# Kernel tuning notes

Hardware: AMD Instinct MI355X
Metric: run time of the kernel (lower is better)

Reference implementation:

```python
import jax, jax.numpy as jnp
import numpy as np

N = 100000   # nodes per layer
E = 600000   # edges per block
FIN = 256    # raw feature dim
H = 128      # hidden_size
C = 47       # n_classes
L = 3        # num_layers = n_layers + 1
NOUT = 10000 # seed nodes
GEN_EPS = 1e-7
T = 1.0
LN_EPS = 1e-5


def setup_inputs() -> dict:
    key = jax.random.key(0)
    ks = jax.random.split(key, 10)
    return {
        "x": jax.random.normal(ks[0], (N, FIN), jnp.float32),
        "src": jax.random.randint(ks[1], (L - 1, E), 0, N),
        "dst": jax.random.randint(ks[2], (L - 1, E), 0, N),
        "node_map": jax.random.randint(ks[3], (L - 1, N), 0, N),
        "final_map": jax.random.randint(ks[4], (NOUT,), 0, N),
        "enc_w": jax.random.normal(ks[5], (FIN, H), jnp.float32) * 0.05,
        "enc_b": jnp.zeros((H,), jnp.float32),
        "gcn_w": jax.random.normal(ks[6], (L, H, H), jnp.float32) * 0.05,
        "gcn_b": jnp.zeros((L, H), jnp.float32),
        "ln_g": jnp.ones((L, H), jnp.float32),
        "ln_b": jnp.zeros((L, H), jnp.float32),
        "pred_w": jax.random.normal(ks[7], (H, C), jnp.float32) * 0.05,
        "pred_b": jnp.zeros((C,), jnp.float32),
    }


def _layer_norm(h, g, b):
    mu = jnp.mean(h, axis=-1, keepdims=True)
    var = jnp.mean(jnp.square(h - mu), axis=-1, keepdims=True)
    return (h - mu) * jax.lax.rsqrt(var + LN_EPS) * g + b


def _gen_conv(h, src, dst, w, b):
    # GENConv, aggr='softmax', mlp_layers=1, no edge_attr, no msg_norm.
    m = jax.nn.relu(h[src]) + GEN_EPS                      # [E, H] messages
    # per-destination, per-feature segment softmax with temperature T
    mx = jax.ops.segment_max(m * T, dst, num_segments=N)   # [N, H]
    e = jnp.exp(m * T - mx[dst])                           # [E, H]
    denom = jax.ops.segment_sum(e, dst, num_segments=N)    # [N, H]
    alpha = e / (denom[dst] + 1e-16)
    agg = jax.ops.segment_sum(m * alpha, dst, num_segments=N)  # [N, H]
    return (agg + h) @ w + b                               # residual + Linear (MLP)


def reference(x, src, dst, node_map, final_map, enc_w, enc_b,
              gcn_w, gcn_b, ln_g, ln_b, pred_w, pred_b):
    h = x @ enc_w + enc_b                                  # node_features_encoder
    h = _gen_conv(h, src[0], dst[0], gcn_w[0], gcn_b[0])   # gcns[0] with block-0 edges
    for layer in range(1, L):                              # res+ block
        h2 = jax.nn.relu(_layer_norm(h, ln_g[layer - 1], ln_b[layer - 1]))
        # dropout is identity in eval mode (p applied with training=False)
        # gcns[layer] uses the edge_index set BEFORE this iteration's move
        h = _gen_conv(h2, src[layer - 1], dst[layer - 1],
                      gcn_w[layer], gcn_b[layer]) + h
        h = h[node_map[layer - 1]]                         # nf_move_layer_to gather
    h = jax.nn.relu(_layer_norm(h, ln_g[L - 1], ln_b[L - 1]))
    h = h @ pred_w + pred_b                                # node_pred_linear
    h = h[final_map]                                       # seed-node extraction
    return jax.nn.log_softmax(h, axis=-1)
```

## Files before the change

kernel.cpp:

```cpp
#include <hip/hip_runtime.h>
#include <hip/hip_bf16.h>
#include <hip/hip_fp16.h>

typedef unsigned short u16;
typedef unsigned int u32;

#define N_NODES 100000
#define N_EDGES 600000
#define FIN_D   256
#define HDIM    128
#define NCLS    47
#define NOUT_D  10000
#define NCHUNK  196
#define NP2     100352
#define PCH     2048
#define PNB     ((N_EDGES + PCH - 1) / PCH)
#define EB      1024

typedef short bf16x8 __attribute__((ext_vector_type(8)));
typedef float f32x4  __attribute__((ext_vector_type(4)));

#define GPTR(p) (const __attribute__((address_space(1))) u32*)(p)
#define LPTR(p) (__attribute__((address_space(3))) u32*)(p)

__device__ __forceinline__ float bf2f(u16 u) {
    union { u32 i; float f; } v; v.i = ((u32)u) << 16; return v.f;
}
__device__ __forceinline__ u16 f2bf(float f) {
    __hip_bfloat16 h = __float2bfloat16(f);
    return *reinterpret_cast<u16*>(&h);
}
__device__ __forceinline__ float loadF(const void* p, size_t i, bool f32) {
    if (f32) return ((const float*)p)[i];
    return bf2f(((const u16*)p)[i]);
}
__device__ __forceinline__ float wave_sum(float v) {
    #pragma unroll
    for (int o = 32; o > 0; o >>= 1) v += __shfl_xor(v, o, 64);
    return v;
}
__device__ __forceinline__ float wave_max(float v) {
    #pragma unroll
    for (int o = 32; o > 0; o >>= 1) v = fmaxf(v, __shfl_xor(v, o, 64));
    return v;
}
__device__ __forceinline__ int block_excl_scan_256(int v, int* wsum) {
    int lane = threadIdx.x & 63, wv = threadIdx.x >> 6;
    int inc = v;
    #pragma unroll
    for (int off = 1; off < 64; off <<= 1) {
        int u = __shfl_up(inc, off, 64);
        if (lane >= off) inc += u;
    }
    if (lane == 63) wsum[wv] = inc;
    __syncthreads();
    if (threadIdx.x == 0) {
        int a = 0;
        #pragma unroll
        for (int w = 0; w < 4; ++w) { int t = wsum[w]; wsum[w] = a; a += t; }
    }
    __syncthreads();
    return inc - v + wsum[wv];
}

__global__ __launch_bounds__(256) void dtype_detect_kernel(
    const u16* __restrict__ x, int* __restrict__ flag)
{
    int i = blockIdx.x * 256 + threadIdx.x;
    u32 e = (x[i] >> 7) & 0xFF;
    unsigned long long b = __ballot(e >= 200);
    if ((threadIdx.x & 63) == 0) {
        int c = __popcll(b);
        if (c) atomicAdd(&flag[1], c);
    }
}

__global__ __launch_bounds__(256) void histb_kernel(
    const int* __restrict__ dst, int* __restrict__ bcnt, int ebgrid)
{
    __shared__ int h[NCHUNK];
    int half = (blockIdx.x >= ebgrid) ? 1 : 0;
    int e0 = (blockIdx.x - half * ebgrid) * EB;
    for (int i = threadIdx.x; i < NCHUNK; i += 256) h[i] = 0;
    __syncthreads();
    #pragma unroll
    for (int t = 0; t < 4; ++t) {
        int e = e0 + t * 256 + threadIdx.x;
        if (e < N_EDGES) atomicAdd(&h[dst[half * N_EDGES + e] >> 9], 1);
    }
    __syncthreads();
    for (int i = threadIdx.x; i < NCHUNK; i += 256)
        if (h[i]) atomicAdd(&bcnt[half * NCHUNK + i], h[i]);
}

__global__ __launch_bounds__(256) void coff2_kernel(
    const int* __restrict__ csum, int* __restrict__ coff,
    int* __restrict__ bcur)
{
    __shared__ int wsum[4];
    int t = threadIdx.x;
    for (int h = 0; h < 2; ++h) {
        int v = (t < NCHUNK) ? csum[h * NCHUNK + t] : 0;
        int excl = block_excl_scan_256(v, wsum);
        if (t < NCHUNK) {
            coff[h * NCHUNK + t] = excl;
            bcur[(h * NCHUNK + t) * 16] = excl;
        }
        __syncthreads();
    }
}

__global__ __launch_bounds__(256) void bucket_part_kernel(
    const int* __restrict__ src, const int* __restrict__ dst,
    const int* __restrict__ comp1,
    int* __restrict__ bcur, int2* __restrict__ tmp,
    int* __restrict__ deg2)
{
    __shared__ int hist[NCHUNK];
    __shared__ int base[NCHUNK];
    int half = (blockIdx.x >= PNB) ? 1 : 0;
    int b = blockIdx.x - half * PNB;
    int e0 = b * PCH;
    for (int i = threadIdx.x; i < NCHUNK; i += 256) hist[i] = 0;
    __syncthreads();

    int2 loc[8];
    #pragma unroll
    for (int t = 0; t < 8; ++t) {
        int e = e0 + t * 256 + threadIdx.x;
        loc[t].y = -1;
        if (e < N_EDGES) {
            int ge = half * N_EDGES + e;
            int d = dst[ge];
            int s = src[ge];
            if (half) s = comp1[s];
            loc[t] = make_int2(s, d);
            atomicAdd(&hist[d >> 9], 1);
            atomicAdd(&deg2[half * NP2 + d], 1);
        }
    }
    __syncthreads();
    for (int i = threadIdx.x; i < NCHUNK; i += 256) {
        int h = hist[i];
        base[i] = (h > 0) ? atomicAdd(&bcur[(half * NCHUNK + i) * 16], h) : 0;
        hist[i] = 0;
    }
    __syncthreads();
    #pragma unroll
    for (int t = 0; t < 8; ++t) {
        if (loc[t].y >= 0) {
            int bk = loc[t].y >> 9;
            int pos = base[bk] + atomicAdd(&hist[bk], 1);
            tmp[(size_t)half * N_EDGES + pos] = loc[t];
        }
    }
}

__global__ __launch_bounds__(256) void scan2_kernel(
    const int* __restrict__ deg2, const int* __restrict__ coff,
    int* __restrict__ rp0, int* __restrict__ rp1)
{
    __shared__ int wsum[4];
    int half = (blockIdx.x >= NCHUNK) ? 1 : 0;
    int b = blockIdx.x - half * NCHUNK;
    const int* deg = deg2 + half * NP2;
    int* rp = half ? rp1 : rp0;
    int t = threadIdx.x;
    int i0 = b * 512 + 2 * t;
    int d0 = (i0 < N_NODES) ? deg[i0] : 0;
    int d1 = (i0 + 1 < N_NODES) ? deg[i0 + 1] : 0;
    int excl = block_excl_scan_256(d0 + d1, wsum);
    int base = coff[half * NCHUNK + b] + excl;
    if (i0 < N_NODES)     rp[i0] = base;
    if (i0 + 1 < N_NODES) rp[i0 + 1] = base + d0;
    if (b == 0 && t == 0) rp[N_NODES] = N_EDGES;
}

__global__ __launch_bounds__(256) void bucket_sort_kernel(
    const int2* __restrict__ tmp,
    const int* __restrict__ rp0, const int* __restrict__ rp1,
    const int* __restrict__ coff, const int* __restrict__ csum,
    int* __restrict__ ei0, int* __restrict__ ei1)
{
    __shared__ int cur[512];
    int half = (blockIdx.x >= NCHUNK) ? 1 : 0;
    int b = blockIdx.x - half * NCHUNK;
    const int* rp = half ? rp1 : rp0;
    int* ei = half ? ei1 : ei0;
    int n0 = b * 512;
    #pragma unroll
    for (int i = threadIdx.x; i < 512; i += 256) {
        int n = n0 + i;
        cur[i] = (n < N_NODES) ? rp[n] : 0;
    }
    __syncthreads();
    int beg = coff[half * NCHUNK + b];
    int end = beg + csum[half * NCHUNK + b];
    for (int i = beg + threadIdx.x; i < end; i += 256) {
        int2 p = tmp[(size_t)half * N_EDGES + i];
        int pos = atomicAdd(&cur[p.y & 511], 1);
        ei[pos] = p.x;
    }
}

__global__ __launch_bounds__(256) void pack_b_kernel(
    const void* __restrict__ enc_w, const void* __restrict__ gcn_w,
    const int* __restrict__ dt, u16* __restrict__ Bp)
{
    const bool f32 = (dt[1] > 16);
    int o = blockIdx.x * 256 + threadIdx.x;
    if (o >= 32768 + 3 * 16384) return;
    const void* srcp; size_t soff; int m;
    if (o < 32768) { srcp = enc_w; soff = 0; m = o; }
    else {
        int l = (o - 32768) >> 14;
        srcp = gcn_w; soff = (size_t)l * 16384; m = (o - 32768) & 16383;
    }
    int j    = m & 7;
    int lane = (m >> 3) & 63;
    int ct   = (m >> 9) & 7;
    int kidx = m >> 12;
    int k = kidx * 32 + (lane >> 4) * 8 + j;
    int n = ct * 16 + (lane & 15);
    Bp[o] = f2bf(loadF(srcp, soff + (size_t)k * HDIM + n, f32));
}

__global__ __launch_bounds__(256, 2) void enc_gemm_kernel(
    const void* __restrict__ Araw, const u16* __restrict__ Bp,
    const void* __restrict__ bias, const int* __restrict__ dt,
    u16* __restrict__ OutBF)
{
    extern __shared__ char SH[];
    const bool f32 = (dt[1] > 16);
    const int tid  = threadIdx.x;
    const int w    = tid >> 6;
    const int lane = tid & 63;
    const int quad = lane >> 4;
    const int cl   = lane & 15;
    const int m0   = blockIdx.x * 16;

    #pragma unroll
    for (int i = 0; i < 16; ++i) {
        int off = (w * 16 + i) * 1024;
        __builtin_amdgcn_global_load_lds(
            GPTR((const char*)Bp + off + lane * 16),
            LPTR(SH + off), 16, 0, 0);
    }
    if (f32) {
        #pragma unroll
        for (int i = 0; i < 4; ++i) {
            int row = w * 4 + i;
            int src = (lane * 16) ^ ((row & 7) << 4);
            __builtin_amdgcn_global_load_lds(
                GPTR((const char*)Araw + (size_t)(m0 + row) * 1024 + src),
                LPTR(SH + 65536 + row * 1024), 16, 0, 0);
        }
    } else {
        #pragma unroll
        for (int i = 0; i < 2; ++i) {
            int r0 = (w * 2 + i) * 2;
            int row = r0 + (lane >> 5);
            int src = ((lane & 31) * 16) ^ ((row & 7) << 4);
            __builtin_amdgcn_global_load_lds(
                GPTR((const char*)Araw + (size_t)(m0 + row) * 512 + src),
                LPTR(SH + 65536 + r0 * 512), 16, 0, 0);
        }
    }

    f32x4 acc[2];
    acc[0] = (f32x4){0.f, 0.f, 0.f, 0.f};
    acc[1] = (f32x4){0.f, 0.f, 0.f, 0.f};
    const int ct0 = w * 2;
    const int swz = (cl & 7) << 4;

    __syncthreads();

    #pragma unroll
    for (int k = 0; k < 8; ++k) {
        bf16x8 av;
        if (f32) {
            const char* rb = SH + 65536 + cl * 1024;
            int lo = (k * 128 + quad * 32) ^ swz;
            float4 v0 = *(const float4*)(rb + lo);
            float4 v1 = *(const float4*)(rb + (lo ^ 16));
            union { u32 u[4]; bf16x8 v; } cv;
            cv.u[0] = (u32)f2bf(v0.x) | ((u32)f2bf(v0.y) << 16);
            cv.u[1] = (u32)f2bf(v0.z) | ((u32)f2bf(v0.w) << 16);
            cv.u[2] = (u32)f2bf(v1.x) | ((u32)f2bf(v1.y) << 16);
            cv.u[3] = (u32)f2bf(v1.z) | ((u32)f2bf(v1.w) << 16);
            av = cv.v;
        } else {
            const char* rb = SH + 65536 + cl * 512;
            av = *(const bf16x8*)(rb + ((k * 64 + quad * 16) ^ swz));
        }
        #pragma unroll
        for (int c = 0; c < 2; ++c) {
            bf16x8 b = *(const bf16x8*)(SH + k * 8192 + (ct0 + c) * 1024 + lane * 16);
            acc[c] = __builtin_amdgcn_mfma_f32_16x16x32_bf16(av, b, acc[c], 0, 0, 0);
        }
    }

    #pragma unroll
    for (int reg = 0; reg < 4; ++reg) {
        int grow = m0 + quad * 4 + reg;
        #pragma unroll
        for (int c = 0; c < 2; ++c) {
            int col = (ct0 + c) * 16 + cl;
            float v = acc[c][reg] + loadF(bias, col, f32);
            OutBF[(size_t)grow * HDIM + col] = f2bf(v);
        }
    }
}

template<bool OWN_MAP>
__global__ __launch_bounds__(256) void agg_msg_kernel(
    const int* __restrict__ rp, const int* __restrict__ eidx,
    const u16* __restrict__ HBin, const int* __restrict__ own_map,
    u16* __restrict__ Amsg)
{
    __shared__ u32 RS[4][16][64];
    int wave = threadIdx.x >> 6;
    int lane = threadIdx.x & 63;
    int n = blockIdx.x * 4 + wave;
    if (n >= N_NODES) return;
    const u32* HB32 = (const u32*)HBin;
    int nn = OWN_MAP ? own_map[n] : n;
    u32 own = HB32[(size_t)nn * 64 + lane];
    int beg = rp[n], end = rp[n + 1];
    float den0 = 0.f, den1 = 0.f, num0 = 0.f, num1 = 0.f;
    for (int c = beg; c < end; c += 16) {
        int cnt = end - c; if (cnt > 16) cnt = 16;
        int e = c + (lane & 15); if (e > end - 1) e = end - 1;
        int ei = eidx[e];
        int nI = (cnt + 3) >> 2;
        #pragma unroll
        for (int i = 0; i < 4; ++i) {
            if (i < nI) {
                int s = __shfl(ei, i * 4 + (lane >> 4), 64);
                __builtin_amdgcn_global_load_lds(
                    GPTR((const char*)HBin + (size_t)s * 256 + (lane & 15) * 16),
                    LPTR(&RS[wave][i * 4][0]), 16, 0, 0);
            }
        }
        asm volatile("s_waitcnt vmcnt(0)" ::: "memory");
        __builtin_amdgcn_sched_barrier(0);
        #pragma unroll
        for (int t = 0; t < 16; ++t) {
            if (t >= cnt) break;
            u32 h = RS[wave][t][lane];
            float m0 = fmaxf(bf2f((u16)(h & 0xffff)), 0.f) + 1e-7f;
            float m1 = fmaxf(bf2f((u16)(h >> 16)),    0.f) + 1e-7f;
            float e0 = __expf(m0), e1 = __expf(m1);
            den0 += e0; num0 += m0 * e0;
            den1 += e1; num1 += m1 * e1;
        }
        asm volatile("s_waitcnt lgkmcnt(0)" ::: "memory");
        __builtin_amdgcn_sched_barrier(0);
    }
    float a0 = num0 / (den0 + 1e-16f) + bf2f((u16)(own & 0xffff));
    float a1 = num1 / (den1 + 1e-16f) + bf2f((u16)(own >> 16));
    ((u32*)Amsg)[(size_t)n * 64 + lane] = (u32)f2bf(a0) | ((u32)f2bf(a1) << 16);
}

template<bool RES, bool OWN_MAP, bool WRITE_LN>
__global__ __launch_bounds__(256) void conv_gemm_kernel(
    const u16* __restrict__ Amsg, const int* __restrict__ own_map,
    const u16* __restrict__ Bp, int Bpbase,
    const void* __restrict__ bias, int biasoff,
    const __half* __restrict__ Resid,
    const void* __restrict__ lng, const void* __restrict__ lnb, int lnoff,
    const int* __restrict__ dt,
    __half* __restrict__ OutH, u16* __restrict__ HBout)
{
    const bool f32 = (dt[1] > 16);
    __shared__ u16 Bsh[16384];
    __shared__ u16 Ash[8192];
    const int tid  = threadIdx.x;
    const int w    = tid >> 6;
    const int lane = tid & 63;
    const int quad = lane >> 4;
    const int cl   = lane & 15;
    const int m0   = blockIdx.x * 64;

    {
        const char* Bp2 = (const char*)(Bp + Bpbase);
        #pragma unroll
        for (int i = 0; i < 8; ++i)
            __builtin_amdgcn_global_load_lds(
                GPTR(Bp2 + i * 4096 + w * 1024 + lane * 16),
                LPTR((char*)Bsh + i * 4096 + w * 1024), 16, 0, 0);
        const char* Ab = (const char*)Amsg + (size_t)m0 * 256;
        #pragma unroll
        for (int i = 0; i < 4; ++i) {
            int row_local = i * 16 + w * 4 + (lane >> 4);
            int off = ((lane & 15) * 16) ^ ((row_local & 7) << 4);
            __builtin_amdgcn_global_load_lds(
                GPTR(Ab + (size_t)row_local * 256 + off),
                LPTR((char*)Ash + i * 4096 + w * 1024), 16, 0, 0);
        }
    }

    __syncthreads();

    const int row_local = w * 16 + cl;
    const char* ar = (const char*)Ash + row_local * 256;
    const int akey = (row_local & 7) << 4;
    bf16x8 afr[4];
    #pragma unroll
    for (int kidx = 0; kidx < 4; ++kidx)
        afr[kidx] = *(const bf16x8*)(ar + ((kidx * 64 + quad * 16) ^ akey));

    f32x4 acc[8];
    #pragma unroll
    for (int ct = 0; ct < 8; ++ct) acc[ct] = (f32x4){0.f, 0.f, 0.f, 0.f};
    #pragma unroll
    for (int kidx = 0; kidx < 4; ++kidx) {
        const u16* bb = Bsh + ((size_t)(kidx * 8) * 64 + lane) * 8;
        #pragma unroll
        for (int ct = 0; ct < 8; ++ct) {
            bf16x8 b = *(const bf16x8*)(bb + (size_t)ct * 512);
            acc[ct] = __builtin_amdgcn_mfma_f32_16x16x32_bf16(afr[kidx], b, acc[ct], 0, 0, 0);
        }
    }

    #pragma unroll
    for (int reg = 0; reg < 4; ++reg) {
        int n = m0 + w * 16 + quad * 4 + reg;
        if (n >= N_NODES) continue;
        size_t rrow = 0;
        if (RES) rrow = (size_t)(OWN_MAP ? own_map[n] : n) * HDIM;
        float v[8];
        float s1 = 0.f, s2 = 0.f;
        #pragma unroll
        for (int ct = 0; ct < 8; ++ct) {
            int col = ct * 16 + cl;
            float x = acc[ct][reg] + loadF(bias, biasoff + col, f32);
            if (RES) x += __half2float(Resid[rrow + col]);
            v[ct] = x;
            OutH[(size_t)n * HDIM + col] = __float2half(x);
            s1 += x; s2 += x * x;
        }
        if (WRITE_LN) {
            #pragma unroll
            for (int o = 1; o < 16; o <<= 1) {
                s1 += __shfl_xor(s1, o, 64);
                s2 += __shfl_xor(s2, o, 64);
            }
            float mu = s1 * (1.0f / 128.0f);
            float var = s2 * (1.0f / 128.0f) - mu * mu;
            float rs = rsqrtf(fmaxf(var, 0.f) + 1e-5f);
            #pragma unroll
            for (int ct = 0; ct < 8; ++ct) {
                int col = ct * 16 + cl;
                float y = fmaxf((v[ct] - mu) * rs * loadF(lng, lnoff + col, f32)
                                + loadF(lnb, lnoff + col, f32), 0.f);
                HBout[(size_t)n * HDIM + col] = f2bf(y);
            }
        }
    }
}

__global__ __launch_bounds__(256) void final_head_kernel(
    const __half* __restrict__ Hsrc, const int* __restrict__ map1,
    const int* __restrict__ fmap,
    const void* __restrict__ g, const void* __restrict__ b, int goff,
    const void* __restrict__ pw, const void* __restrict__ pb,
    const int* __restrict__ dt, void* __restrict__ out)
{
    const bool f32 = (dt[1] > 16);
    __shared__ float pwl[HDIM * 48];
    __shared__ float pbl[64];
    __shared__ float sh[4][HDIM];
    const int tid = threadIdx.x, wave = tid >> 6, lane = tid & 63;

    for (int i = tid; i < HDIM * NCLS; i += 256)
        pwl[(i / NCLS) * 48 + (i % NCLS)] = loadF(pw, i, f32);
    if (tid < NCLS) pbl[tid] = loadF(pb, tid, f32);
    __syncthreads();

    int i = blockIdx.x * 4 + wave;
    int jj = map1[fmap[i]];
    __half2 hv = *((const __half2*)(Hsrc + (size_t)jj * HDIM) + lane);
    float2 v = __half22float2(hv);
    float mu = wave_sum(v.x + v.y) * (1.0f / 128.0f);
    float d0 = v.x - mu, d1 = v.y - mu;
    float var = wave_sum(d0 * d0 + d1 * d1) * (1.0f / 128.0f);
    float rs = rsqrtf(var + 1e-5f);
    int f0 = lane * 2;
    sh[wave][f0]     = fmaxf(d0 * rs * loadF(g, goff + f0, f32)     + loadF(b, goff + f0, f32),     0.0f);
    sh[wave][f0 + 1] = fmaxf(d1 * rs * loadF(g, goff + f0 + 1, f32) + loadF(b, goff + f0 + 1, f32), 0.0f);
    float acc = -1e30f;
    if (lane < NCLS) {
        acc = pbl[lane];
        #pragma unroll 8
        for (int k = 0; k < HDIM; ++k)
            acc = fmaf(sh[wave][k], pwl[k * 48 + lane], acc);
    }
    float mx = wave_max(acc);
    float ex = (lane < NCLS) ? __expf(acc - mx) : 0.0f;
    float sum = wave_sum(ex);
    if (lane < NCLS) {
        float r = acc - mx - logf(sum);
        if (f32) ((float*)out)[(size_t)i * NCLS + lane] = r;
        else     ((u16*)out)[(size_t)i * NCLS + lane] = f2bf(r);
    }
}

extern "C" void kernel_launch(void* const* d_in, const int* in_sizes, int n_in,
                              void* d_out, int out_size, void* d_ws, size_t ws_size,
                              hipStream_t stream) {
    const void* x       = d_in[0];
    const int* src      = (const int*)d_in[1];
    const int* dst      = (const int*)d_in[2];
    const int* node_map = (const int*)d_in[3];
    const int* fmap     = (const int*)d_in[4];
    const void* enc_w   = d_in[5];
    const void* enc_b   = d_in[6];
    const void* gcn_w   = d_in[7];
    const void* gcn_b   = d_in[8];
    const void* ln_g    = d_in[9];
    const void* ln_b    = d_in[10];
    const void* pred_w  = d_in[11];
    const void* pred_b  = d_in[12];

    char* ws = (char*)d_ws;
    const size_t szH = (size_t)N_NODES * HDIM * sizeof(u16);
    __half* Pa  = (__half*)ws;  ws += szH;
    __half* Pb  = (__half*)ws;  ws += szH;
    u16*   HBa  = (u16*)ws;     ws += szH;
    u16*   HBb  = (u16*)ws;     ws += szH;
    u16*   Amsg = (u16*)ws;     ws += szH;
    int*   FLAG = (int*)ws;     ws += 1024;
    u16*   Bp   = (u16*)ws;     ws += (size_t)(32768 + 3 * 16384) * 2 + 1024;
    int*  deg2  = (int*)ws;  ws += (size_t)2 * NP2 * 4;
    int*  rp0   = (int*)ws;  ws += (size_t)(N_NODES + 2) * 4;
    int*  rp1   = (int*)ws;  ws += (size_t)(N_NODES + 2) * 4;
    int*  ei0   = (int*)ws;  ws += (size_t)N_EDGES * 4;
    int*  ei1   = (int*)ws;  ws += (size_t)N_EDGES * 4;
    int2* tmp   = (int2*)ws; ws += (size_t)2 * N_EDGES * 8;
    int*  csum  = (int*)ws;  ws += 2048;
    int*  coff  = (int*)ws;  ws += 2048;
    int*  bcur  = (int*)ws;  ws += (size_t)2 * NCHUNK * 16 * 4 + 1024;

    dim3 blk(256);
    const int ggrid = (N_NODES + 63) / 64;
    const int g16   = (N_NODES + 15) / 16;
    const int ebgrid = (N_EDGES + EB - 1) / EB;
    const int agrid = (N_NODES + 3) / 4;
    const int pgrid = (32768 + 3 * 16384 + 255) / 256;

    hipMemsetAsync(FLAG, 0, 64, stream);
    hipMemsetAsync(csum, 0, 2048 * sizeof(int), stream);
    dtype_detect_kernel<<<256, blk, 0, stream>>>((const u16*)x, FLAG);
    pack_b_kernel<<<pgrid, blk, 0, stream>>>(enc_w, gcn_w, FLAG, Bp);

    hipMemsetAsync(deg2, 0, (size_t)2 * NP2 * 4, stream);
    histb_kernel<<<2 * ebgrid, blk, 0, stream>>>(dst, csum, ebgrid);
    coff2_kernel<<<1, blk, 0, stream>>>(csum, coff, bcur);
    bucket_part_kernel<<<2 * PNB, blk, 0, stream>>>(src, dst, node_map, bcur, tmp,
                                                    deg2);
    scan2_kernel<<<2 * NCHUNK, blk, 0, stream>>>(deg2, coff, rp0, rp1);
    bucket_sort_kernel<<<2 * NCHUNK, blk, 0, stream>>>(tmp, rp0, rp1, coff, csum,
                                                       ei0, ei1);

    enc_gemm_kernel<<<g16, blk, 81920, stream>>>(x, Bp, enc_b, FLAG, HBa);

    agg_msg_kernel<false><<<agrid, blk, 0, stream>>>(rp0, ei0, HBa, nullptr, Amsg);
    conv_gemm_kernel<false, false, true><<<ggrid, blk, 0, stream>>>(
        Amsg, nullptr, Bp, 32768, gcn_b, 0, nullptr,
        ln_g, ln_b, 0, FLAG, Pa, HBb);

    agg_msg_kernel<false><<<agrid, blk, 0, stream>>>(rp0, ei0, HBb, nullptr, Amsg);
    conv_gemm_kernel<true, false, true><<<ggrid, blk, 0, stream>>>(
        Amsg, nullptr, Bp, 32768 + 16384, gcn_b, 128, Pa,
        ln_g, ln_b, 128, FLAG, Pb, HBa);

    agg_msg_kernel<true><<<agrid, blk, 0, stream>>>(rp1, ei1, HBa, node_map, Amsg);
    conv_gemm_kernel<true, true, false><<<ggrid, blk, 0, stream>>>(
        Amsg, node_map, Bp, 32768 + 2 * 16384, gcn_b, 256, Pb,
        ln_g, ln_b, 256, FLAG, Pa, nullptr);

    final_head_kernel<<<NOUT_D / 4, blk, 0, stream>>>(
        Pa, node_map + N_NODES, fmap, ln_g, ln_b, 256, pred_w, pred_b, FLAG,
        (void*)d_out);
}
```

Baseline: 588.4 us.

## Fuse degree count and row-pointer scan into bucket sort using LDS

Per-node in-degrees are no longer accumulated with global atomics in the partition kernel. Each bucket-sort block now counts the degrees of its 512-node chunk in shared memory, scans them, writes the row pointers and then scatters the edges. This removes the deg2 buffer and its memset, a whole kernel launch, and about a million global atomics. In exchange, each bucket-sort block reads its slice of the temporary edge array twice.

Result: faster. 543.5 us (-7.6%).

```diff
diff --git a/kernel.cpp b/kernel.cpp
--- a/kernel.cpp
+++ b/kernel.cpp
@@ -113,8 +113,7 @@
 __global__ __launch_bounds__(256) void bucket_part_kernel(
     const int* __restrict__ src, const int* __restrict__ dst,
     const int* __restrict__ comp1,
-    int* __restrict__ bcur, int2* __restrict__ tmp,
-    int* __restrict__ deg2)
+    int* __restrict__ bcur, int2* __restrict__ tmp)
 {
     __shared__ int hist[NCHUNK];
     __shared__ int base[NCHUNK];
@@ -136,7 +135,6 @@
             if (half) s = comp1[s];
             loc[t] = make_int2(s, d);
             atomicAdd(&hist[d >> 9], 1);
-            atomicAdd(&deg2[half * NP2 + d], 1);
         }
     }
     __syncthreads();
@@ -156,47 +154,39 @@
     }
 }
 
-__global__ __launch_bounds__(256) void scan2_kernel(
-    const int* __restrict__ deg2, const int* __restrict__ coff,
-    int* __restrict__ rp0, int* __restrict__ rp1)
-{
+__global__ __launch_bounds__(256) void bucket_sort_kernel(
+    const int2* __restrict__ tmp,
+    const int* __restrict__ coff, const int* __restrict__ csum,
+    int* __restrict__ rp0, int* __restrict__ rp1,
+    int* __restrict__ ei0, int* __restrict__ ei1)
+{
+    __shared__ int cur[512];
     __shared__ int wsum[4];
     int half = (blockIdx.x >= NCHUNK) ? 1 : 0;
     int b = blockIdx.x - half * NCHUNK;
-    const int* deg = deg2 + half * NP2;
     int* rp = half ? rp1 : rp0;
-    int t = threadIdx.x;
-    int i0 = b * 512 + 2 * t;
-    int d0 = (i0 < N_NODES) ? deg[i0] : 0;
-    int d1 = (i0 + 1 < N_NODES) ? deg[i0 + 1] : 0;
-    int excl = block_excl_scan_256(d0 + d1, wsum);
-    int base = coff[half * NCHUNK + b] + excl;
-    if (i0 < N_NODES)     rp[i0] = base;
-    if (i0 + 1 < N_NODES) rp[i0 + 1] = base + d0;
-    if (b == 0 && t == 0) rp[N_NODES] = N_EDGES;
-}
-
-__global__ __launch_bounds__(256) void bucket_sort_kernel(
-    const int2* __restrict__ tmp,
-    const int* __restrict__ rp0, const int* __restrict__ rp1,
-    const int* __restrict__ coff, const int* __restrict__ csum,
-    int* __restrict__ ei0, int* __restrict__ ei1)
-{
-    __shared__ int cur[512];
-    int half = (blockIdx.x >= NCHUNK) ? 1 : 0;
-    int b = blockIdx.x - half * NCHUNK;
-    const int* rp = half ? rp1 : rp0;
     int* ei = half ? ei1 : ei0;
     int n0 = b * 512;
-    #pragma unroll
-    for (int i = threadIdx.x; i < 512; i += 256) {
-        int n = n0 + i;
-        cur[i] = (n < N_NODES) ? rp[n] : 0;
-    }
-    __syncthreads();
     int beg = coff[half * NCHUNK + b];
     int end = beg + csum[half * NCHUNK + b];
-    for (int i = beg + threadIdx.x; i < end; i += 256) {
+    const int t = threadIdx.x;
+
+    cur[t] = 0; cur[t + 256] = 0;
+    __syncthreads();
+    for (int i = beg + t; i < end; i += 256)
+        atomicAdd(&cur[tmp[(size_t)half * N_EDGES + i].y & 511], 1);
+    __syncthreads();
+
+    int d0 = cur[2 * t], d1 = cur[2 * t + 1];
+    int excl = block_excl_scan_256(d0 + d1, wsum);
+    int base = beg + excl;
+    cur[2 * t] = base;
+    cur[2 * t + 1] = base + d0;
+    if (n0 + 2 * t <= N_NODES)     rp[n0 + 2 * t] = base;
+    if (n0 + 2 * t + 1 <= N_NODES) rp[n0 + 2 * t + 1] = base + d0;
+    __syncthreads();
+
+    for (int i = beg + t; i < end; i += 256) {
         int2 p = tmp[(size_t)half * N_EDGES + i];
         int pos = atomicAdd(&cur[p.y & 511], 1);
         ei[pos] = p.x;
@@ -532,7 +522,6 @@
     u16*   Amsg = (u16*)ws;     ws += szH;
     int*   FLAG = (int*)ws;     ws += 1024;
     u16*   Bp   = (u16*)ws;     ws += (size_t)(32768 + 3 * 16384) * 2 + 1024;
-    int*  deg2  = (int*)ws;  ws += (size_t)2 * NP2 * 4;
     int*  rp0   = (int*)ws;  ws += (size_t)(N_NODES + 2) * 4;
     int*  rp1   = (int*)ws;  ws += (size_t)(N_NODES + 2) * 4;
     int*  ei0   = (int*)ws;  ws += (size_t)N_EDGES * 4;
@@ -550,18 +539,15 @@
     const int pgrid = (32768 + 3 * 16384 + 255) / 256;
 
     hipMemsetAsync(FLAG, 0, 64, stream);
-    hipMemsetAsync(csum, 0, 2048 * sizeof(int), stream);
+    hipMemsetAsync(csum, 0, 2048, stream);
     dtype_detect_kernel<<<256, blk, 0, stream>>>((const u16*)x, FLAG);
     pack_b_kernel<<<pgrid, blk, 0, stream>>>(enc_w, gcn_w, FLAG, Bp);
 
-    hipMemsetAsync(deg2, 0, (size_t)2 * NP2 * 4, stream);
     histb_kernel<<<2 * ebgrid, blk, 0, stream>>>(dst, csum, ebgrid);
     coff2_kernel<<<1, blk, 0, stream>>>(csum, coff, bcur);
-    bucket_part_kernel<<<2 * PNB, blk, 0, stream>>>(src, dst, node_map, bcur, tmp,
-                                                    deg2);
-    scan2_kernel<<<2 * NCHUNK, blk, 0, stream>>>(deg2, coff, rp0, rp1);
-    bucket_sort_kernel<<<2 * NCHUNK, blk, 0, stream>>>(tmp, rp0, rp1, coff, csum,
-                                                       ei0, ei1);
+    bucket_part_kernel<<<2 * PNB, blk, 0, stream>>>(src, dst, node_map, bcur, tmp);
+    bucket_sort_kernel<<<2 * NCHUNK, blk, 0, stream>>>(tmp, coff, csum,
+                                                       rp0, rp1, ei0, ei1);
 
     enc_gemm_kernel<<<g16, blk, 81920, stream>>>(x, Bp, enc_b, FLAG, HBa);
 
```
